# Kernel tuning notes

Hardware: AMD Instinct MI355X
Metric: run time of the kernel (lower is better)

Reference implementation:

```python
import jax, jax.numpy as jnp
import numpy as np

B, N, M12, H, O, I, DIFF = 8192, 100, 12, 64, 128, 12, 1.0
TWO_PI = 2.0 * np.pi


def _moments_single(xi, K):
    # xi: [N, 2] single sample; K: [12, 2] exponent pairs -> [12]
    xc = xi - xi.mean(axis=0)                 # center per-sample (mean over points)
    p = xc[:, None, :] ** K[None, :, :]       # [N, 12, 2]
    return jnp.sum(p[..., 0] * p[..., 1], axis=0)  # [12]


def setup_inputs() -> dict:
    key = jax.random.key(0)
    ks = jax.random.split(key, 8)
    # 12 integer central-moment exponent pairs (p, q)
    P = jnp.array([1, 2, 0, 2, 1, 3, 0, 2, 3, 1, 4, 0], jnp.float32)
    Q = jnp.array([1, 0, 2, 1, 2, 0, 3, 2, 1, 3, 0, 4], jnp.float32)
    K = jnp.stack([P, Q], axis=-1)            # [12, 2]

    x = jax.random.normal(ks[0], (B, N, 2), jnp.float32)
    t = jax.random.uniform(ks[1], (1,), jnp.float32, 0.1, 1.0)  # positive time
    W_fourier = jax.random.normal(ks[2], (H // 2,), jnp.float32) * 30.0

    def lin(k, fin, fout):
        bound = 1.0 / np.sqrt(fin)
        kw, kb = jax.random.split(k)
        W = jax.random.uniform(kw, (fin, fout), jnp.float32, -bound, bound)
        b = jax.random.uniform(kb, (fout,), jnp.float32, -bound, bound)
        return W, b

    embed_W, embed_b = lin(ks[3], H, H)
    lin1_W, lin1_b = lin(ks[4], I, H)
    lin2a_W, lin2a_b = lin(ks[5], H, O)
    lin2b_W, lin2b_b = lin(ks[6], O, I)
    lin2c_W, lin2c_b = lin(ks[7], I, I)
    return {
        'x': x, 't': t, 'K': K, 'W_fourier': W_fourier,
        'embed_W': embed_W, 'embed_b': embed_b,
        'lin1_W': lin1_W, 'lin1_b': lin1_b,
        'lin2a_W': lin2a_W, 'lin2a_b': lin2a_b,
        'lin2b_W': lin2b_W, 'lin2b_b': lin2b_b,
        'lin2c_W': lin2c_W, 'lin2c_b': lin2c_b,
    }


def reference(x, t, K, W_fourier, embed_W, embed_b, lin1_W, lin1_b,
              lin2a_W, lin2a_b, lin2b_W, lin2b_b, lin2c_W, lin2c_b):
    # Invariance encoding ('Moment' mode): [B, 12]
    m = jax.vmap(_moments_single, in_axes=(0, None))(x, K)
    h = jax.nn.gelu(m @ lin1_W + lin1_b, approximate=False)   # [B, H] (dropout = eval identity)
    # Gaussian Fourier time embedding: [1, H]
    xp = t[:, None] * W_fourier[None, :] * TWO_PI
    emb = jnp.concatenate([jnp.sin(xp), jnp.cos(xp)], axis=-1) @ embed_W + embed_b
    h = jax.nn.gelu((h + emb) @ lin2a_W + lin2a_b, approximate=False)
    h = jax.nn.gelu(h @ lin2b_W + lin2b_b, approximate=False)
    h = (h @ lin2c_W + lin2c_b) / jnp.sqrt(DIFF * t)          # [B, 12]
    # Per-sample jacobian of the moment map: [B, 12, N, 2]
    # (equals the block diagonal of torch.autograd.functional.jacobian over the batch)
    jac = jax.vmap(jax.jacrev(_moments_single), in_axes=(0, None))(x, K)
    # Replaces the (i, j) double loop of tiny matmuls with one batched contraction
    return jnp.einsum('bk,bknj->bnj', h, jac)                 # [B, N, 2]
```

## Files before the change

### kernel.cpp

```cpp
#include <hip/hip_runtime.h>
#include <hip/hip_bf16.h>


static __device__ __forceinline__ float gelu_f(float x) {
    float y = 0.7071067811865475f * x;
    float s = fabsf(y);
    float t = __builtin_amdgcn_rcpf(fmaf(0.3275911f, s, 1.0f));
    float p = t * fmaf(t, fmaf(t, fmaf(t, fmaf(t, 1.061405429f,
                    -1.453152027f), 1.421413741f), -0.284496736f), 0.254829592f);
    float e = __expf(-y * y);
    float ea = fmaf(-p, e, 1.0f);
    float erfv = copysignf(ea, y);
    return 0.5f * x * (1.0f + erfv);
}

#define DPP_ADD(v, ctrl) \
    v += __int_as_float(__builtin_amdgcn_update_dpp(0, __float_as_int(v), ctrl, 0xf, 0xf, true))

static __device__ __forceinline__ float wave_sum(float v) {
    DPP_ADD(v, 0x111);
    DPP_ADD(v, 0x112);
    DPP_ADD(v, 0x114);
    DPP_ADD(v, 0x118);
    DPP_ADD(v, 0x142);
    DPP_ADD(v, 0x143);
    return __int_as_float(__builtin_amdgcn_readlane(__float_as_int(v), 63));
}

#define TWO_PI_F 6.283185307179586f

__global__ __launch_bounds__(256, 4) void scorenet_fused(
    const float* __restrict__ x,
    const float* __restrict__ t_in,
    const float* __restrict__ Wf,
    const float* __restrict__ embW,
    const float* __restrict__ embB,
    const float* __restrict__ W1,
    const float* __restrict__ b1,
    const float* __restrict__ W2a,
    const float* __restrict__ b2a,
    const float* __restrict__ W2b,
    const float* __restrict__ b2b,
    const float* __restrict__ W2c,
    const float* __restrict__ b2c,
    float* __restrict__ out,
    int B)
{
    __shared__ float s_f[64];
    __shared__ float s_emb[64];

    const int tid = threadIdx.x;
    const float tval = t_in[0];

    if (tid < 32) {
        float xp = tval * Wf[tid] * TWO_PI_F;
        s_f[tid]      = sinf(xp);
        s_f[tid + 32] = cosf(xp);
    }
    __syncthreads();
    if (tid < 64) {
        float acc = embB[tid];
        const float4* f4 = reinterpret_cast<const float4*>(s_f);
        #pragma unroll
        for (int c = 0; c < 16; ++c) {
            float4 a4 = f4[c];
            int j = 4 * c;
            acc = fmaf(a4.x, embW[(j+0)*64 + tid],
                  fmaf(a4.y, embW[(j+1)*64 + tid],
                  fmaf(a4.z, embW[(j+2)*64 + tid],
                  fmaf(a4.w, embW[(j+3)*64 + tid], acc))));
        }
        s_emb[tid] = acc;
    }
    __syncthreads();

    const int lane = tid & 63;
    const int b = blockIdx.x * 4 + (tid >> 6);
    if (b >= B) return;

    const float2* px = reinterpret_cast<const float2*>(x) + (size_t)b * 100;
    const bool has2 = lane < 36;

    float2 p0 = px[lane];
    float2 p1 = px[has2 ? lane + 64 : lane];

    float wb[24];
    {
        const float4* w2b4 = reinterpret_cast<const float4*>(W2b + lane * 24);
        #pragma unroll
        for (int c = 0; c < 6; ++c) {
            float4 q = w2b4[c];
            wb[4*c+0] = q.x; wb[4*c+1] = q.y; wb[4*c+2] = q.z; wb[4*c+3] = q.w;
        }
    }

    float xa = p0.x, ya = p0.y;
    float xb = has2 ? p1.x : 0.0f;
    float yb = has2 ? p1.y : 0.0f;

    const float mux = wave_sum(xa + xb) * 0.01f;
    const float muy = wave_sum(ya + yb) * 0.01f;

    float ua = xa - mux, va = ya - muy;
    float ub = has2 ? (xb - mux) : 0.0f;
    float vb = has2 ? (yb - muy) : 0.0f;

    float ms[12];
    {
        float u2 = ua * ua, v2 = va * va;
        ms[0] = ua * va;   ms[1] = u2;        ms[2] = v2;
        ms[3] = u2 * va;   ms[4] = ua * v2;
        ms[5] = u2 * ua;   ms[6] = v2 * va;
        ms[7] = u2 * v2;   ms[8] = ms[5] * va; ms[9] = ua * ms[6];
        ms[10] = u2 * u2;  ms[11] = v2 * v2;
        float w2 = ub * ub, z2 = vb * vb;
        ms[0] += ub * vb;  ms[1] += w2;       ms[2] += z2;
        ms[3] += w2 * vb;  ms[4] += ub * z2;
        ms[5] += w2 * ub;  ms[6] += z2 * vb;
        ms[7] += w2 * z2;  ms[8] += w2 * ub * vb; ms[9] += ub * z2 * vb;
        ms[10] += w2 * w2; ms[11] += z2 * z2;
    }
    float m[12];
    #pragma unroll
    for (int k = 0; k < 12; ++k) m[k] = wave_sum(ms[k]);

    float a1 = b1[lane];
    #pragma unroll
    for (int k = 0; k < 12; ++k) a1 = fmaf(m[k], W1[k * 64 + lane], a1);
    float aval = gelu_f(a1) + s_emb[lane];

    const float2* w2a2 = reinterpret_cast<const float2*>(W2a);
    float accE0 = b2a[2 * lane], accO0 = b2a[2 * lane + 1];
    float accE1 = 0.0f, accO1 = 0.0f;
    #pragma unroll
    for (int j = 0; j < 64; j += 2) {
        float aj0 = __int_as_float(__builtin_amdgcn_readlane(__float_as_int(aval), j));
        float aj1 = __int_as_float(__builtin_amdgcn_readlane(__float_as_int(aval), j + 1));
        float2 w0 = w2a2[(size_t)j * 64 + lane];
        float2 w1v = w2a2[(size_t)(j + 1) * 64 + lane];
        accE0 = fmaf(aj0, w0.x, accE0);
        accO0 = fmaf(aj0, w0.y, accO0);
        accE1 = fmaf(aj1, w1v.x, accE1);
        accO1 = fmaf(aj1, w1v.y, accO1);
    }
    float h2e = gelu_f(accE0 + accE1);
    float h2o = gelu_f(accO0 + accO1);

    float h3[12];
    #pragma unroll
    for (int k = 0; k < 12; ++k) {
        float p3 = fmaf(h2e, wb[k], h2o * wb[12 + k]);
        h3[k] = gelu_f(wave_sum(p3) + b2b[k]);
    }

    const float rst = rsqrtf(tval);
    float h[12];
    #pragma unroll
    for (int k = 0; k < 12; ++k) {
        float acc = b2c[k];
        #pragma unroll
        for (int j = 0; j < 12; ++j) acc = fmaf(h3[j], W2c[j * 12 + k], acc);
        h[k] = acc * rst;
    }

    const float inv_n = 0.01f;
    float c0 = (2.0f*h[3]*m[0] + h[4]*m[2] + 3.0f*h[5]*m[1] + 2.0f*h[7]*m[4]
              + 3.0f*h[8]*m[3] + h[9]*m[6] + 4.0f*h[10]*m[5]) * inv_n;
    float c1 = (h[3]*m[1] + 2.0f*h[4]*m[0] + 3.0f*h[6]*m[2] + 2.0f*h[7]*m[3]
              + h[8]*m[5] + 3.0f*h[9]*m[4] + 4.0f*h[11]*m[6]) * inv_n;

    const float A1 = 2.0f*h[1], A2 = h[0],      A3 = 3.0f*h[5], A4 = 2.0f*h[3], A5 = h[4];
    const float A6 = 4.0f*h[10],A7 = 3.0f*h[8], A8 = 2.0f*h[7], A9 = h[9];
    const float B1 = h[0],      B2 = 2.0f*h[2], B3 = h[3],      B4 = 2.0f*h[4], B5 = 3.0f*h[6];
    const float B6 = h[8],      B7 = 2.0f*h[7], B8 = 3.0f*h[9], B9 = 4.0f*h[11];

    float2* pout = reinterpret_cast<float2*>(out) + (size_t)b * 100;
    {
        float u = ua, v = va;
        float u2 = u*u, v2 = v*v;
        float o0 = A1*u + A2*v + A3*u2 + A4*u*v + A5*v2 + A6*u2*u + A7*u2*v + A8*u*v2 + A9*v2*v - c0;
        float o1 = B1*u + B2*v + B3*u2 + B4*u*v + B5*v2 + B6*u2*u + B7*u2*v + B8*u*v2 + B9*v2*v - c1;
        float2 r; r.x = o0; r.y = o1;
        pout[lane] = r;
    }
    if (has2) {
        float u = ub, v = vb;
        float u2 = u*u, v2 = v*v;
        float o0 = A1*u + A2*v + A3*u2 + A4*u*v + A5*v2 + A6*u2*u + A7*u2*v + A8*u*v2 + A9*v2*v - c0;
        float o1 = B1*u + B2*v + B3*u2 + B4*u*v + B5*v2 + B6*u2*u + B7*u2*v + B8*u*v2 + B9*v2*v - c1;
        float2 r; r.x = o0; r.y = o1;
        pout[lane + 64] = r;
    }
}

extern "C" void kernel_launch(void* const* d_in, const int* in_sizes, int n_in,
                              void* d_out, int out_size, void* d_ws, size_t ws_size,
                              hipStream_t stream) {
    const float* x    = (const float*)d_in[0];
    const float* t    = (const float*)d_in[1];
    const float* Wf   = (const float*)d_in[3];
    const float* embW = (const float*)d_in[4];
    const float* embB = (const float*)d_in[5];
    const float* W1   = (const float*)d_in[6];
    const float* b1   = (const float*)d_in[7];
    const float* W2a  = (const float*)d_in[8];
    const float* b2a  = (const float*)d_in[9];
    const float* W2b  = (const float*)d_in[10];
    const float* b2b  = (const float*)d_in[11];
    const float* W2c  = (const float*)d_in[12];
    const float* b2c  = (const float*)d_in[13];

    const int B = in_sizes[0] / 200;
    const int blocks = (B + 3) / 4;

    scorenet_fused<<<blocks, 256, 0, stream>>>(
        x, t, Wf, embW, embB, W1, b1, W2a, b2a, W2b, b2b, W2c, b2c,
        (float*)d_out, B);
}
```

Before: 104.2 us.

## Stage all MLP weights in LDS and process four samples per wave

Each block now copies W2a, W2b, W1, W2c and the biases into shared memory once, then every wave handles four samples in a loop instead of one. Per-lane weight slices are kept in registers, and the final 12x12 layer is spread across lanes and broadcast with readlane rather than computed redundantly by every lane. The aim is to spread the embedding and weight-load setup over more samples and to serve the 64x128 matmul from LDS instead of global or L2. The cost is about 43KB of LDS per block, lower occupancy (launch bounds 2), fewer blocks, and a serial per-sample loop inside each wave.

```diff
diff --git a/kernel.cpp b/kernel.cpp
--- a/kernel.cpp
+++ b/kernel.cpp
@@ -27,9 +27,14 @@
     return __int_as_float(__builtin_amdgcn_readlane(__float_as_int(v), 63));
 }
 
+static __device__ __forceinline__ float bcast_lane(float v, int l) {
+    return __int_as_float(__builtin_amdgcn_readlane(__float_as_int(v), l));
+}
+
 #define TWO_PI_F 6.283185307179586f
-
-__global__ __launch_bounds__(256, 4) void scorenet_fused(
+#define SAMPLES_PER_BLOCK 16
+
+__global__ __launch_bounds__(256, 2) void scorenet_fused(
     const float* __restrict__ x,
     const float* __restrict__ t_in,
     const float* __restrict__ Wf,
@@ -46,18 +51,36 @@
     float* __restrict__ out,
     int B)
 {
-    __shared__ float s_f[64];
+    __shared__ __align__(16) float s_W2a[8192];
+    __shared__ __align__(16) float s_W2b[1536];
+    __shared__ __align__(16) float s_W1[768];
+    __shared__ __align__(16) float s_W2c[144];
+    __shared__ __align__(16) float s_b1[64];
+    __shared__ __align__(16) float s_b2a[128];
+    __shared__ __align__(16) float s_b2b[12];
+    __shared__ __align__(16) float s_b2c[12];
+    __shared__ __align__(16) float s_f[64];
     __shared__ float s_emb[64];
 
     const int tid = threadIdx.x;
     const float tval = t_in[0];
 
-    if (tid < 32) {
-        float xp = tval * Wf[tid] * TWO_PI_F;
-        s_f[tid]      = sinf(xp);
-        s_f[tid + 32] = cosf(xp);
+    for (int i = tid; i < 2048; i += 256) ((float4*)s_W2a)[i] = ((const float4*)W2a)[i];
+    for (int i = tid; i < 384;  i += 256) ((float4*)s_W2b)[i] = ((const float4*)W2b)[i];
+    for (int i = tid; i < 192;  i += 256) ((float4*)s_W1)[i]  = ((const float4*)W1)[i];
+    for (int i = tid; i < 36;   i += 256) ((float4*)s_W2c)[i] = ((const float4*)W2c)[i];
+    for (int i = tid; i < 16;   i += 256) ((float4*)s_b1)[i]  = ((const float4*)b1)[i];
+    for (int i = tid; i < 32;   i += 256) ((float4*)s_b2a)[i] = ((const float4*)b2a)[i];
+    for (int i = tid; i < 3;    i += 256) ((float4*)s_b2b)[i] = ((const float4*)b2b)[i];
+    for (int i = tid; i < 3;    i += 256) ((float4*)s_b2c)[i] = ((const float4*)b2c)[i];
+    if (tid >= 224) {
+        int i = tid - 224;
+        float xp = tval * Wf[i] * TWO_PI_F;
+        s_f[i]      = sinf(xp);
+        s_f[i + 32] = cosf(xp);
     }
     __syncthreads();
+
     if (tid < 64) {
         float acc = embB[tid];
         const float4* f4 = reinterpret_cast<const float4*>(s_f);
@@ -75,121 +98,139 @@
     __syncthreads();
 
     const int lane = tid & 63;
-    const int b = blockIdx.x * 4 + (tid >> 6);
-    if (b >= B) return;
-
-    const float2* px = reinterpret_cast<const float2*>(x) + (size_t)b * 100;
+    const int wv = tid >> 6;
     const bool has2 = lane < 36;
 
-    float2 p0 = px[lane];
-    float2 p1 = px[has2 ? lane + 64 : lane];
-
     float wb[24];
-    {
-        const float4* w2b4 = reinterpret_cast<const float4*>(W2b + lane * 24);
-        #pragma unroll
-        for (int c = 0; c < 6; ++c) {
-            float4 q = w2b4[c];
-            wb[4*c+0] = q.x; wb[4*c+1] = q.y; wb[4*c+2] = q.z; wb[4*c+3] = q.w;
-        }
-    }
-
-    float xa = p0.x, ya = p0.y;
-    float xb = has2 ? p1.x : 0.0f;
-    float yb = has2 ? p1.y : 0.0f;
-
-    const float mux = wave_sum(xa + xb) * 0.01f;
-    const float muy = wave_sum(ya + yb) * 0.01f;
-
-    float ua = xa - mux, va = ya - muy;
-    float ub = has2 ? (xb - mux) : 0.0f;
-    float vb = has2 ? (yb - muy) : 0.0f;
-
-    float ms[12];
-    {
-        float u2 = ua * ua, v2 = va * va;
-        ms[0] = ua * va;   ms[1] = u2;        ms[2] = v2;
-        ms[3] = u2 * va;   ms[4] = ua * v2;
-        ms[5] = u2 * ua;   ms[6] = v2 * va;
-        ms[7] = u2 * v2;   ms[8] = ms[5] * va; ms[9] = ua * ms[6];
-        ms[10] = u2 * u2;  ms[11] = v2 * v2;
-        float w2 = ub * ub, z2 = vb * vb;
-        ms[0] += ub * vb;  ms[1] += w2;       ms[2] += z2;
-        ms[3] += w2 * vb;  ms[4] += ub * z2;
-        ms[5] += w2 * ub;  ms[6] += z2 * vb;
-        ms[7] += w2 * z2;  ms[8] += w2 * ub * vb; ms[9] += ub * z2 * vb;
-        ms[10] += w2 * w2; ms[11] += z2 * z2;
-    }
-    float m[12];
-    #pragma unroll
-    for (int k = 0; k < 12; ++k) m[k] = wave_sum(ms[k]);
-
-    float a1 = b1[lane];
-    #pragma unroll
-    for (int k = 0; k < 12; ++k) a1 = fmaf(m[k], W1[k * 64 + lane], a1);
-    float aval = gelu_f(a1) + s_emb[lane];
-
-    const float2* w2a2 = reinterpret_cast<const float2*>(W2a);
-    float accE0 = b2a[2 * lane], accO0 = b2a[2 * lane + 1];
-    float accE1 = 0.0f, accO1 = 0.0f;
-    #pragma unroll
-    for (int j = 0; j < 64; j += 2) {
-        float aj0 = __int_as_float(__builtin_amdgcn_readlane(__float_as_int(aval), j));
-        float aj1 = __int_as_float(__builtin_amdgcn_readlane(__float_as_int(aval), j + 1));
-        float2 w0 = w2a2[(size_t)j * 64 + lane];
-        float2 w1v = w2a2[(size_t)(j + 1) * 64 + lane];
-        accE0 = fmaf(aj0, w0.x, accE0);
-        accO0 = fmaf(aj0, w0.y, accO0);
-        accE1 = fmaf(aj1, w1v.x, accE1);
-        accO1 = fmaf(aj1, w1v.y, accO1);
-    }
-    float h2e = gelu_f(accE0 + accE1);
-    float h2o = gelu_f(accO0 + accO1);
-
-    float h3[12];
-    #pragma unroll
-    for (int k = 0; k < 12; ++k) {
-        float p3 = fmaf(h2e, wb[k], h2o * wb[12 + k]);
-        h3[k] = gelu_f(wave_sum(p3) + b2b[k]);
-    }
-
-    const float rst = rsqrtf(tval);
-    float h[12];
-    #pragma unroll
-    for (int k = 0; k < 12; ++k) {
-        float acc = b2c[k];
-        #pragma unroll
-        for (int j = 0; j < 12; ++j) acc = fmaf(h3[j], W2c[j * 12 + k], acc);
-        h[k] = acc * rst;
-    }
-
-    const float inv_n = 0.01f;
-    float c0 = (2.0f*h[3]*m[0] + h[4]*m[2] + 3.0f*h[5]*m[1] + 2.0f*h[7]*m[4]
-              + 3.0f*h[8]*m[3] + h[9]*m[6] + 4.0f*h[10]*m[5]) * inv_n;
-    float c1 = (h[3]*m[1] + 2.0f*h[4]*m[0] + 3.0f*h[6]*m[2] + 2.0f*h[7]*m[3]
-              + h[8]*m[5] + 3.0f*h[9]*m[4] + 4.0f*h[11]*m[6]) * inv_n;
-
-    const float A1 = 2.0f*h[1], A2 = h[0],      A3 = 3.0f*h[5], A4 = 2.0f*h[3], A5 = h[4];
-    const float A6 = 4.0f*h[10],A7 = 3.0f*h[8], A8 = 2.0f*h[7], A9 = h[9];
-    const float B1 = h[0],      B2 = 2.0f*h[2], B3 = h[3],      B4 = 2.0f*h[4], B5 = 3.0f*h[6];
-    const float B6 = h[8],      B7 = 2.0f*h[7], B8 = 3.0f*h[9], B9 = 4.0f*h[11];
-
-    float2* pout = reinterpret_cast<float2*>(out) + (size_t)b * 100;
-    {
-        float u = ua, v = va;
-        float u2 = u*u, v2 = v*v;
-        float o0 = A1*u + A2*v + A3*u2 + A4*u*v + A5*v2 + A6*u2*u + A7*u2*v + A8*u*v2 + A9*v2*v - c0;
-        float o1 = B1*u + B2*v + B3*u2 + B4*u*v + B5*v2 + B6*u2*u + B7*u2*v + B8*u*v2 + B9*v2*v - c1;
-        float2 r; r.x = o0; r.y = o1;
-        pout[lane] = r;
-    }
-    if (has2) {
-        float u = ub, v = vb;
-        float u2 = u*u, v2 = v*v;
-        float o0 = A1*u + A2*v + A3*u2 + A4*u*v + A5*v2 + A6*u2*u + A7*u2*v + A8*u*v2 + A9*v2*v - c0;
-        float o1 = B1*u + B2*v + B3*u2 + B4*u*v + B5*v2 + B6*u2*u + B7*u2*v + B8*u*v2 + B9*v2*v - c1;
-        float2 r; r.x = o0; r.y = o1;
-        pout[lane + 64] = r;
+    #pragma unroll
+    for (int k = 0; k < 24; ++k) wb[k] = s_W2b[lane * 24 + k];
+    float w1c[12];
+    #pragma unroll
+    for (int k = 0; k < 12; ++k) w1c[k] = s_W1[k * 64 + lane];
+    float b2bv[12];
+    #pragma unroll
+    for (int k = 0; k < 12; ++k) b2bv[k] = s_b2b[k];
+    const int kk = lane < 12 ? lane : 0;
+    float w2ck[12];
+    #pragma unroll
+    for (int j = 0; j < 12; ++j) w2ck[j] = s_W2c[j * 12 + kk];
+    const float b2ck = s_b2c[kk];
+    const float b1v  = s_b1[lane];
+    const float b2aE = s_b2a[2 * lane], b2aO = s_b2a[2 * lane + 1];
+    const float embv = s_emb[lane];
+    const float rst  = rsqrtf(tval);
+
+    const int b0 = blockIdx.x * SAMPLES_PER_BLOCK + wv * 4;
+
+    float2 P0[4], P1[4];
+    #pragma unroll
+    for (int s = 0; s < 4; ++s) {
+        int bs = b0 + s; if (bs >= B) bs = B - 1;
+        const float2* px = reinterpret_cast<const float2*>(x) + (size_t)bs * 100;
+        P0[s] = px[lane];
+        P1[s] = px[has2 ? lane + 64 : lane];
+    }
+
+    for (int s = 0; s < 4; ++s) {
+        const int b = b0 + s;
+
+        float xa = P0[s].x, ya = P0[s].y;
+        float xb = has2 ? P1[s].x : 0.0f;
+        float yb = has2 ? P1[s].y : 0.0f;
+
+        const float mux = wave_sum(xa + xb) * 0.01f;
+        const float muy = wave_sum(ya + yb) * 0.01f;
+
+        float ua = xa - mux, va = ya - muy;
+        float ub = has2 ? (xb - mux) : 0.0f;
+        float vb = has2 ? (yb - muy) : 0.0f;
+
+        float ms[12];
+        {
+            float u2 = ua * ua, v2 = va * va;
+            ms[0] = ua * va;   ms[1] = u2;        ms[2] = v2;
+            ms[3] = u2 * va;   ms[4] = ua * v2;
+            ms[5] = u2 * ua;   ms[6] = v2 * va;
+            ms[7] = u2 * v2;   ms[8] = ms[5] * va; ms[9] = ua * ms[6];
+            ms[10] = u2 * u2;  ms[11] = v2 * v2;
+            float w2 = ub * ub, z2 = vb * vb;
+            ms[0] += ub * vb;  ms[1] += w2;       ms[2] += z2;
+            ms[3] += w2 * vb;  ms[4] += ub * z2;
+            ms[5] += w2 * ub;  ms[6] += z2 * vb;
+            ms[7] += w2 * z2;  ms[8] += w2 * ub * vb; ms[9] += ub * z2 * vb;
+            ms[10] += w2 * w2; ms[11] += z2 * z2;
+        }
+        float m[12];
+        #pragma unroll
+        for (int k = 0; k < 12; ++k) m[k] = wave_sum(ms[k]);
+
+        float a1 = b1v;
+        #pragma unroll
+        for (int k = 0; k < 12; ++k) a1 = fmaf(m[k], w1c[k], a1);
+        float aval = gelu_f(a1) + embv;
+
+        const float2* w2a2 = reinterpret_cast<const float2*>(s_W2a);
+        float accE0 = b2aE, accO0 = b2aO;
+        float accE1 = 0.0f, accO1 = 0.0f;
+        #pragma unroll
+        for (int j = 0; j < 64; j += 2) {
+            float aj0 = bcast_lane(aval, j);
+            float aj1 = bcast_lane(aval, j + 1);
+            float2 w0  = w2a2[j * 64 + lane];
+            float2 w1v = w2a2[(j + 1) * 64 + lane];
+            accE0 = fmaf(aj0, w0.x,  accE0);
+            accO0 = fmaf(aj0, w0.y,  accO0);
+            accE1 = fmaf(aj1, w1v.x, accE1);
+            accO1 = fmaf(aj1, w1v.y, accO1);
+        }
+        float h2e = gelu_f(accE0 + accE1);
+        float h2o = gelu_f(accO0 + accO1);
+
+        float h3[12];
+        #pragma unroll
+        for (int k = 0; k < 12; ++k) {
+            float p3 = fmaf(h2e, wb[k], h2o * wb[12 + k]);
+            h3[k] = gelu_f(wave_sum(p3) + b2bv[k]);
+        }
+
+        float acch = b2ck;
+        #pragma unroll
+        for (int j = 0; j < 12; ++j) acch = fmaf(h3[j], w2ck[j], acch);
+        acch *= rst;
+        float h[12];
+        #pragma unroll
+        for (int k = 0; k < 12; ++k) h[k] = bcast_lane(acch, k);
+
+        const float inv_n = 0.01f;
+        float c0 = (2.0f*h[3]*m[0] + h[4]*m[2] + 3.0f*h[5]*m[1] + 2.0f*h[7]*m[4]
+                  + 3.0f*h[8]*m[3] + h[9]*m[6] + 4.0f*h[10]*m[5]) * inv_n;
+        float c1 = (h[3]*m[1] + 2.0f*h[4]*m[0] + 3.0f*h[6]*m[2] + 2.0f*h[7]*m[3]
+                  + h[8]*m[5] + 3.0f*h[9]*m[4] + 4.0f*h[11]*m[6]) * inv_n;
+
+        const float A1 = 2.0f*h[1], A2 = h[0],      A3 = 3.0f*h[5], A4 = 2.0f*h[3], A5 = h[4];
+        const float A6 = 4.0f*h[10],A7 = 3.0f*h[8], A8 = 2.0f*h[7], A9 = h[9];
+        const float B1 = h[0],      B2 = 2.0f*h[2], B3 = h[3],      B4 = 2.0f*h[4], B5 = 3.0f*h[6];
+        const float B6 = h[8],      B7 = 2.0f*h[7], B8 = 3.0f*h[9], B9 = 4.0f*h[11];
+
+        if (b < B) {
+            float2* pout = reinterpret_cast<float2*>(out) + (size_t)b * 100;
+            {
+                float u = ua, v = va;
+                float u2 = u*u, v2 = v*v;
+                float o0 = A1*u + A2*v + A3*u2 + A4*u*v + A5*v2 + A6*u2*u + A7*u2*v + A8*u*v2 + A9*v2*v - c0;
+                float o1 = B1*u + B2*v + B3*u2 + B4*u*v + B5*v2 + B6*u2*u + B7*u2*v + B8*u*v2 + B9*v2*v - c1;
+                float2 r; r.x = o0; r.y = o1;
+                pout[lane] = r;
+            }
+            if (has2) {
+                float u = ub, v = vb;
+                float u2 = u*u, v2 = v*v;
+                float o0 = A1*u + A2*v + A3*u2 + A4*u*v + A5*v2 + A6*u2*u + A7*u2*v + A8*u*v2 + A9*v2*v - c0;
+                float o1 = B1*u + B2*v + B3*u2 + B4*u*v + B5*v2 + B6*u2*u + B7*u2*v + B8*u*v2 + B9*v2*v - c1;
+                float2 r; r.x = o0; r.y = o1;
+                pout[lane + 64] = r;
+            }
+        }
     }
 }
 
@@ -211,7 +252,7 @@
     const float* b2c  = (const float*)d_in[13];
 
     const int B = in_sizes[0] / 200;
-    const int blocks = (B + 3) / 4;
+    const int blocks = (B + SAMPLES_PER_BLOCK - 1) / SAMPLES_PER_BLOCK;
 
     scorenet_fused<<<blocks, 256, 0, stream>>>(
         x, t, Wf, embW, embB, W1, b1, W2a, b2a, W2b, b2b, W2c, b2c,
```

Result: slower. 125.4 us (+20.4%).
